# Optimization experiments

Measured on AMD Instinct MI355X. Metric: run time of the kernel, lower is better.

The kernel has to match this reference:

```python
import jax, jax.numpy as jnp
import numpy as np

MEX_C = 2.0 / (np.sqrt(3.0) * np.pi ** 0.25)

def mexican_hat(z):
    return MEX_C * (z * z - 1.0) * jnp.exp(-0.5 * z * z)

def setup_inputs() -> dict:
    key = jax.random.key(0)
    ks = jax.random.split(key, 5)
    B, T, D, O = 4, 2048, 128, 128
    x = jax.random.normal(ks[0], (B, T, D), dtype=jnp.float32)
    # init like torch: scale ~ U(0.5,1.5), translation ~ U(-0.5,0.5), kaiming-ish weights
    scale = jax.random.uniform(ks[1], (O, D), dtype=jnp.float32, minval=0.5, maxval=1.5)
    translation = jax.random.uniform(ks[2], (O, D), dtype=jnp.float32, minval=-0.5, maxval=0.5)
    bound = 1.0 / np.sqrt(D)
    wavelet_weights = jax.random.uniform(ks[3], (O, D), dtype=jnp.float32, minval=-bound, maxval=bound)
    base_w = jax.random.uniform(ks[4], (O, D), dtype=jnp.float32, minval=-bound, maxval=bound)
    ln_gamma = jnp.ones((D,), dtype=jnp.float32)
    ln_beta = jnp.zeros((D,), dtype=jnp.float32)
    return {"x": x, "scale": scale, "translation": translation,
            "wavelet_weights": wavelet_weights, "base_w": base_w,
            "ln_gamma": ln_gamma, "ln_beta": ln_beta}

def reference(x, scale, translation, wavelet_weights, base_w, ln_gamma, ln_beta):
    B, T, D = x.shape
    O = wavelet_weights.shape[0]
    # LayerNorm over last dim (eps = 1e-5, torch default)
    mu = jnp.mean(x, axis=-1, keepdims=True)
    var = jnp.mean((x - mu) ** 2, axis=-1, keepdims=True)
    x_norm = (x - mu) / jnp.sqrt(var + 1e-5) * ln_gamma + ln_beta
    x_flat = x_norm.reshape(B * T, D)                      # (N, D)
    s = jax.nn.softplus(scale) + 0.1                       # (O, D)
    # broadcast intermediate (N, O, D) — the memory-bound path
    z = (x_flat[:, None, :] - translation[None]) / s[None]
    w = jnp.clip(mexican_hat(z), -10.0, 10.0)              # (N, O, D)
    wavelet_out = jnp.einsum('nod,od->no', w, wavelet_weights)
    base_out = x.reshape(B * T, D) @ base_w.T              # base uses raw x
    out = wavelet_out + jax.nn.silu(base_out)
    return out.reshape(B, T, O)
```

## Files before the change

kernel.cpp:

```cpp
#include <hip/hip_runtime.h>


#define D_DIM 128
#define O_DIM 128
#define ROWS  8
#define BLOCK 256
#define CHUNK 16
#define NCHUNK (D_DIM / CHUNK)

#define C1     0.72134752f
#define SQRT_C 0.84932180f
#define WWK    1.2023651f
#define LOG2E  1.44269504f

typedef float v2f __attribute__((ext_vector_type(2)));

__device__ __forceinline__ float4 wk_transform(float sc, float tr, float w_w, float b_w) {
    float sp  = fmaxf(sc, 0.0f) + __logf(1.0f + __expf(-fabsf(sc)));
    float is2 = SQRT_C / (sp + 0.1f);
    float4 w;
    w.x = tr * is2;
    w.y = is2;
    w.z = w_w * WWK;
    w.w = b_w;
    return w;
}

__global__ __launch_bounds__(256) void wavekan_prep(
    const float* __restrict__ scale,
    const float* __restrict__ trans,
    const float* __restrict__ ww,
    const float* __restrict__ bw,
    float4* __restrict__ wsW)
{
    int idx = blockIdx.x * blockDim.x + threadIdx.x;
    if (idx >= O_DIM * D_DIM) return;
    int o = idx >> 7;
    int d = idx & (D_DIM - 1);
    wsW[d * O_DIM + o] = wk_transform(scale[idx], trans[idx], ww[idx], bw[idx]);
}

template<bool USE_WS>
__global__ __launch_bounds__(BLOCK, 4) void wavekan_main(
    const float* __restrict__ x,
    const float* __restrict__ scale,
    const float* __restrict__ trans,
    const float* __restrict__ ww,
    const float* __restrict__ bw,
    const float* __restrict__ gamma,
    const float* __restrict__ beta,
    const float4* __restrict__ wsW,
    float* __restrict__ out,
    int N)
{
    __shared__ float4 s_ln4[D_DIM * 2];
    __shared__ float4 s_rw4[D_DIM * 2];
    __shared__ float4 s_w[CHUNK * O_DIM];

    const int tid  = threadIdx.x;
    const int row0 = blockIdx.x * ROWS;

    {
        const int r  = tid >> 5;
        const int j  = tid & 31;
        const int d0 = j * 4;
        const int grow = row0 + r;

        float4 v4 = make_float4(0.f, 0.f, 0.f, 0.f);
        if (grow < N)
            v4 = *reinterpret_cast<const float4*>(x + (size_t)grow * D_DIM + d0);

        float sum = (v4.x + v4.y) + (v4.z + v4.w);
        float ssq = (v4.x * v4.x + v4.y * v4.y) + (v4.z * v4.z + v4.w * v4.w);
        #pragma unroll
        for (int m = 1; m < 32; m <<= 1) {
            sum += __shfl_xor(sum, m, 64);
            ssq += __shfl_xor(ssq, m, 64);
        }
        const float mean = sum * (1.0f / D_DIM);
        const float var  = ssq * (1.0f / D_DIM) - mean * mean;
        const float rstd = rsqrtf(var + 1e-5f);

        float4 g4 = *reinterpret_cast<const float4*>(gamma + d0);
        float4 b4 = *reinterpret_cast<const float4*>(beta + d0);

        const int q  = r >> 2;
        const int cw = r & 3;
        const int gx = q ^ (j & 1);

        reinterpret_cast<float*>(&s_ln4[(d0 + 0) * 2 + gx])[cw] = (v4.x - mean) * rstd * g4.x + b4.x;
        reinterpret_cast<float*>(&s_ln4[(d0 + 1) * 2 + gx])[cw] = (v4.y - mean) * rstd * g4.y + b4.y;
        reinterpret_cast<float*>(&s_ln4[(d0 + 2) * 2 + gx])[cw] = (v4.z - mean) * rstd * g4.z + b4.z;
        reinterpret_cast<float*>(&s_ln4[(d0 + 3) * 2 + gx])[cw] = (v4.w - mean) * rstd * g4.w + b4.w;
        reinterpret_cast<float*>(&s_rw4[(d0 + 0) * 2 + gx])[cw] = v4.x;
        reinterpret_cast<float*>(&s_rw4[(d0 + 1) * 2 + gx])[cw] = v4.y;
        reinterpret_cast<float*>(&s_rw4[(d0 + 2) * 2 + gx])[cw] = v4.z;
        reinterpret_cast<float*>(&s_rw4[(d0 + 3) * 2 + gx])[cw] = v4.w;
    }

    const int o = tid & (O_DIM - 1);
    const int g = tid >> 7;

    v2f aw0 = {0.f,0.f}, aw1 = {0.f,0.f};
    v2f ab0 = {0.f,0.f}, ab1 = {0.f,0.f};

    for (int c = 0; c < NCHUNK; ++c) {
        __syncthreads();

        if (USE_WS) {
            #pragma unroll
            for (int k = 0; k < (CHUNK * O_DIM) / BLOCK; ++k)
                s_w[k * BLOCK + tid] = wsW[c * (CHUNK * O_DIM) + k * BLOCK + tid];
        } else {
            const int so = tid & 127;
            const int sq = tid >> 7;
            #pragma unroll
            for (int k = 0; k < 8; ++k) {
                const int dloc = sq * 8 + k;
                const int idx  = so * D_DIM + c * CHUNK + dloc;
                s_w[dloc * O_DIM + so] =
                    wk_transform(scale[idx], trans[idx], ww[idx], bw[idx]);
            }
        }
        __syncthreads();

        #pragma unroll
        for (int dl = 0; dl < CHUNK; ++dl) {
            float4 w  = s_w[dl * O_DIM + o];
            const int di = (c * CHUNK + dl) * 2;
            const int gx = g ^ ((dl >> 2) & 1);
            float4 xl = s_ln4[di + gx];
            float4 xr = s_rw4[di + gx];

            v2f u, qq, e;
            u = (v2f){xl.x, xl.y} * w.y - w.x; qq = u * u;
            e = (v2f){__builtin_amdgcn_exp2f(-qq.x), __builtin_amdgcn_exp2f(-qq.y)};
            aw0 += ((qq - C1) * e) * w.z;
            u = (v2f){xl.z, xl.w} * w.y - w.x; qq = u * u;
            e = (v2f){__builtin_amdgcn_exp2f(-qq.x), __builtin_amdgcn_exp2f(-qq.y)};
            aw1 += ((qq - C1) * e) * w.z;

            ab0 += (v2f){xr.x, xr.y} * w.w;
            ab1 += (v2f){xr.z, xr.w} * w.w;
        }
    }

    {
        const int rb = row0 + g * 4;
        float wavv[4]  = {aw0.x, aw0.y, aw1.x, aw1.y};
        float basev[4] = {ab0.x, ab0.y, ab1.x, ab1.y};
        #pragma unroll
        for (int i = 0; i < 4; ++i) {
            if (rb + i < N) {
                float v   = basev[i];
                float sig = 1.0f / (1.0f + __builtin_amdgcn_exp2f(-LOG2E * v));
                out[(size_t)(rb + i) * O_DIM + o] = wavv[i] + v * sig;
            }
        }
    }
}

extern "C" void kernel_launch(void* const* d_in, const int* in_sizes, int n_in,
                              void* d_out, int out_size, void* d_ws, size_t ws_size,
                              hipStream_t stream) {
    const float* x     = (const float*)d_in[0];
    const float* scale = (const float*)d_in[1];
    const float* trans = (const float*)d_in[2];
    const float* ww    = (const float*)d_in[3];
    const float* bw    = (const float*)d_in[4];
    const float* gamma = (const float*)d_in[5];
    const float* beta  = (const float*)d_in[6];
    float* out = (float*)d_out;

    const int N = in_sizes[0] / D_DIM;
    const int grid = (N + ROWS - 1) / ROWS;

    const size_t ws_needed = (size_t)O_DIM * D_DIM * sizeof(float4);
    if (ws_size >= ws_needed) {
        wavekan_prep<<<(O_DIM * D_DIM + 255) / 256, 256, 0, stream>>>(
            scale, trans, ww, bw, (float4*)d_ws);
        wavekan_main<true><<<grid, BLOCK, 0, stream>>>(
            x, scale, trans, ww, bw, gamma, beta, (const float4*)d_ws, out, N);
    } else {
        wavekan_main<false><<<grid, BLOCK, 0, stream>>>(
            x, scale, trans, ww, bw, gamma, beta, nullptr, out, N);
    }
}
```

Before: 101.3 us.

## Hold per-output weights in registers and split D across lanes with shuffle reduction

The main kernel now keeps each thread's slice of transformed weights (32 d-values for one output) in 32 float4 registers, loaded once. It no longer streams weight chunks through shared memory with two barriers per chunk. Each block processes 32 rows with 512 threads: four lane groups split the D dimension and combine partial sums with cross-lane shuffles. The prep kernel now writes weights in a paired layout. This removes repeated LDS weight traffic and syncs, at the cost of high register pressure (launch bounds lowered to 2 blocks per SM), fewer blocks in the grid and an extra reduction per row.

Result: no change. 101.1 us (-0.1%).

```diff
diff --git a/kernel.cpp b/kernel.cpp
--- a/kernel.cpp
+++ b/kernel.cpp
@@ -3,10 +3,9 @@
 
 #define D_DIM 128
 #define O_DIM 128
-#define ROWS  8
-#define BLOCK 256
-#define CHUNK 16
-#define NCHUNK (D_DIM / CHUNK)
+#define ROWS  32
+#define BLOCK 512
+#define XPAD  289
 
 #define C1     0.72134752f
 #define SQRT_C 0.84932180f
@@ -15,15 +14,11 @@
 
 typedef float v2f __attribute__((ext_vector_type(2)));
 
-__device__ __forceinline__ float4 wk_transform(float sc, float tr, float w_w, float b_w) {
+__device__ __forceinline__ void wk_pair(float sc, float tr, float w_w, float b_w,
+                                        float& wx, float& wy, float& wz, float& wb) {
     float sp  = fmaxf(sc, 0.0f) + __logf(1.0f + __expf(-fabsf(sc)));
     float is2 = SQRT_C / (sp + 0.1f);
-    float4 w;
-    w.x = tr * is2;
-    w.y = is2;
-    w.z = w_w * WWK;
-    w.w = b_w;
-    return w;
+    wx = tr * is2; wy = is2; wz = w_w * WWK; wb = b_w;
 }
 
 __global__ __launch_bounds__(256) void wavekan_prep(
@@ -34,14 +29,19 @@
     float4* __restrict__ wsW)
 {
     int idx = blockIdx.x * blockDim.x + threadIdx.x;
-    if (idx >= O_DIM * D_DIM) return;
-    int o = idx >> 7;
-    int d = idx & (D_DIM - 1);
-    wsW[d * O_DIM + o] = wk_transform(scale[idx], trans[idx], ww[idx], bw[idx]);
+    if (idx >= O_DIM * (D_DIM / 2)) return;
+    int o = idx >> 6;
+    int p = idx & 63;
+    int i0 = o * D_DIM + p * 2;
+    float wx0, wy0, wz0, wb0, wx1, wy1, wz1, wb1;
+    wk_pair(scale[i0],     trans[i0],     ww[i0],     bw[i0],     wx0, wy0, wz0, wb0);
+    wk_pair(scale[i0 + 1], trans[i0 + 1], ww[i0 + 1], bw[i0 + 1], wx1, wy1, wz1, wb1);
+    wsW[(p * O_DIM + o) * 2 + 0] = make_float4(wx0, wx1, wy0, wy1);
+    wsW[(p * O_DIM + o) * 2 + 1] = make_float4(wz0, wz1, wb0, wb1);
 }
 
 template<bool USE_WS>
-__global__ __launch_bounds__(BLOCK, 4) void wavekan_main(
+__global__ __launch_bounds__(BLOCK, 2) void wavekan_main(
     const float* __restrict__ x,
     const float* __restrict__ scale,
     const float* __restrict__ trans,
@@ -53,27 +53,53 @@
     float* __restrict__ out,
     int N)
 {
-    __shared__ float4 s_ln4[D_DIM * 2];
-    __shared__ float4 s_rw4[D_DIM * 2];
-    __shared__ float4 s_w[CHUNK * O_DIM];
+    __shared__ float4 s_ln4[4 * XPAD];
+    __shared__ float4 s_rw4[4 * XPAD];
 
     const int tid  = threadIdx.x;
+    const int lane = tid & 63;
+    const int wv   = tid >> 6;
+    const int o    = wv * 16 + (lane & 15);
+    const int dg   = lane >> 4;
     const int row0 = blockIdx.x * ROWS;
 
+    float4 wA[16], wB[16];
+    if (USE_WS) {
+        #pragma unroll
+        for (int k = 0; k < 16; ++k) {
+            const int p = dg * 16 + k;
+            wA[k] = wsW[(p * O_DIM + o) * 2 + 0];
+            wB[k] = wsW[(p * O_DIM + o) * 2 + 1];
+        }
+    } else {
+        #pragma unroll
+        for (int k = 0; k < 16; ++k) {
+            const int i0 = o * D_DIM + dg * 32 + 2 * k;
+            float wx0, wy0, wz0, wb0, wx1, wy1, wz1, wb1;
+            wk_pair(scale[i0],     trans[i0],     ww[i0],     bw[i0],     wx0, wy0, wz0, wb0);
+            wk_pair(scale[i0 + 1], trans[i0 + 1], ww[i0 + 1], bw[i0 + 1], wx1, wy1, wz1, wb1);
+            wA[k] = make_float4(wx0, wx1, wy0, wy1);
+            wB[k] = make_float4(wz0, wz1, wb0, wb1);
+        }
+    }
+
     {
-        const int r  = tid >> 5;
-        const int j  = tid & 31;
-        const int d0 = j * 4;
+        const int r    = tid >> 4;
+        const int j    = tid & 15;
+        const int d0   = j * 8;
         const int grow = row0 + r;
 
-        float4 v4 = make_float4(0.f, 0.f, 0.f, 0.f);
-        if (grow < N)
-            v4 = *reinterpret_cast<const float4*>(x + (size_t)grow * D_DIM + d0);
-
-        float sum = (v4.x + v4.y) + (v4.z + v4.w);
-        float ssq = (v4.x * v4.x + v4.y * v4.y) + (v4.z * v4.z + v4.w * v4.w);
+        float4 va = make_float4(0.f, 0.f, 0.f, 0.f);
+        float4 vb = make_float4(0.f, 0.f, 0.f, 0.f);
+        if (grow < N) {
+            va = *reinterpret_cast<const float4*>(x + (size_t)grow * D_DIM + d0);
+            vb = *reinterpret_cast<const float4*>(x + (size_t)grow * D_DIM + d0 + 4);
+        }
+        float sum = ((va.x + va.y) + (va.z + va.w)) + ((vb.x + vb.y) + (vb.z + vb.w));
+        float ssq = ((va.x * va.x + va.y * va.y) + (va.z * va.z + va.w * va.w))
+                  + ((vb.x * vb.x + vb.y * vb.y) + (vb.z * vb.z + vb.w * vb.w));
         #pragma unroll
-        for (int m = 1; m < 32; m <<= 1) {
+        for (int m = 1; m < 16; m <<= 1) {
             sum += __shfl_xor(sum, m, 64);
             ssq += __shfl_xor(ssq, m, 64);
         }
@@ -81,81 +107,63 @@
         const float var  = ssq * (1.0f / D_DIM) - mean * mean;
         const float rstd = rsqrtf(var + 1e-5f);
 
-        float4 g4 = *reinterpret_cast<const float4*>(gamma + d0);
-        float4 b4 = *reinterpret_cast<const float4*>(beta + d0);
+        float4 ga = *reinterpret_cast<const float4*>(gamma + d0);
+        float4 gb = *reinterpret_cast<const float4*>(gamma + d0 + 4);
+        float4 ba = *reinterpret_cast<const float4*>(beta + d0);
+        float4 bb = *reinterpret_cast<const float4*>(beta + d0 + 4);
 
-        const int q  = r >> 2;
-        const int cw = r & 3;
-        const int gx = q ^ (j & 1);
+        const int wdg = j >> 2;
+        const int q0  = (j & 3) * 2;
+        const int ib  = wdg * XPAD + r * 9 + q0;
 
-        reinterpret_cast<float*>(&s_ln4[(d0 + 0) * 2 + gx])[cw] = (v4.x - mean) * rstd * g4.x + b4.x;
-        reinterpret_cast<float*>(&s_ln4[(d0 + 1) * 2 + gx])[cw] = (v4.y - mean) * rstd * g4.y + b4.y;
-        reinterpret_cast<float*>(&s_ln4[(d0 + 2) * 2 + gx])[cw] = (v4.z - mean) * rstd * g4.z + b4.z;
-        reinterpret_cast<float*>(&s_ln4[(d0 + 3) * 2 + gx])[cw] = (v4.w - mean) * rstd * g4.w + b4.w;
-        reinterpret_cast<float*>(&s_rw4[(d0 + 0) * 2 + gx])[cw] = v4.x;
-        reinterpret_cast<float*>(&s_rw4[(d0 + 1) * 2 + gx])[cw] = v4.y;
-        reinterpret_cast<float*>(&s_rw4[(d0 + 2) * 2 + gx])[cw] = v4.z;
-        reinterpret_cast<float*>(&s_rw4[(d0 + 3) * 2 + gx])[cw] = v4.w;
+        s_ln4[ib]     = make_float4((va.x - mean) * rstd * ga.x + ba.x,
+                                    (va.y - mean) * rstd * ga.y + ba.y,
+                                    (va.z - mean) * rstd * ga.z + ba.z,
+                                    (va.w - mean) * rstd * ga.w + ba.w);
+        s_ln4[ib + 1] = make_float4((vb.x - mean) * rstd * gb.x + bb.x,
+                                    (vb.y - mean) * rstd * gb.y + bb.y,
+                                    (vb.z - mean) * rstd * gb.z + bb.z,
+                                    (vb.w - mean) * rstd * gb.w + bb.w);
+        s_rw4[ib]     = va;
+        s_rw4[ib + 1] = vb;
     }
+    __syncthreads();
 
-    const int o = tid & (O_DIM - 1);
-    const int g = tid >> 7;
-
-    v2f aw0 = {0.f,0.f}, aw1 = {0.f,0.f};
-    v2f ab0 = {0.f,0.f}, ab1 = {0.f,0.f};
-
-    for (int c = 0; c < NCHUNK; ++c) {
-        __syncthreads();
-
-        if (USE_WS) {
-            #pragma unroll
-            for (int k = 0; k < (CHUNK * O_DIM) / BLOCK; ++k)
-                s_w[k * BLOCK + tid] = wsW[c * (CHUNK * O_DIM) + k * BLOCK + tid];
-        } else {
-            const int so = tid & 127;
-            const int sq = tid >> 7;
-            #pragma unroll
-            for (int k = 0; k < 8; ++k) {
-                const int dloc = sq * 8 + k;
-                const int idx  = so * D_DIM + c * CHUNK + dloc;
-                s_w[dloc * O_DIM + so] =
-                    wk_transform(scale[idx], trans[idx], ww[idx], bw[idx]);
-            }
-        }
-        __syncthreads();
-
+    #pragma unroll 1
+    for (int r = 0; r < ROWS; ++r) {
+        const int xb = dg * XPAD + r * 9;
+        v2f aw = {0.f, 0.f};
+        v2f ab = {0.f, 0.f};
         #pragma unroll
-        for (int dl = 0; dl < CHUNK; ++dl) {
-            float4 w  = s_w[dl * O_DIM + o];
-            const int di = (c * CHUNK + dl) * 2;
-            const int gx = g ^ ((dl >> 2) & 1);
-            float4 xl = s_ln4[di + gx];
-            float4 xr = s_rw4[di + gx];
+        for (int k4 = 0; k4 < 8; ++k4) {
+            float4 xl = s_ln4[xb + k4];
+            float4 xr = s_rw4[xb + k4];
+            float4 a0 = wA[2 * k4],     b0 = wB[2 * k4];
+            float4 a1 = wA[2 * k4 + 1], b1 = wB[2 * k4 + 1];
 
             v2f u, qq, e;
-            u = (v2f){xl.x, xl.y} * w.y - w.x; qq = u * u;
-            e = (v2f){__builtin_amdgcn_exp2f(-qq.x), __builtin_amdgcn_exp2f(-qq.y)};
-            aw0 += ((qq - C1) * e) * w.z;
-            u = (v2f){xl.z, xl.w} * w.y - w.x; qq = u * u;
-            e = (v2f){__builtin_amdgcn_exp2f(-qq.x), __builtin_amdgcn_exp2f(-qq.y)};
-            aw1 += ((qq - C1) * e) * w.z;
+            u  = (v2f){xl.x, xl.y} * (v2f){a0.z, a0.w} - (v2f){a0.x, a0.y};
+            qq = u * u;
+            e  = (v2f){__builtin_amdgcn_exp2f(-qq.x), __builtin_amdgcn_exp2f(-qq.y)};
+            aw += ((qq - C1) * e) * (v2f){b0.x, b0.y};
+            ab += (v2f){xr.x, xr.y} * (v2f){b0.z, b0.w};
 
-            ab0 += (v2f){xr.x, xr.y} * w.w;
-            ab1 += (v2f){xr.z, xr.w} * w.w;
+            u  = (v2f){xl.z, xl.w} * (v2f){a1.z, a1.w} - (v2f){a1.x, a1.y};
+            qq = u * u;
+            e  = (v2f){__builtin_amdgcn_exp2f(-qq.x), __builtin_amdgcn_exp2f(-qq.y)};
+            aw += ((qq - C1) * e) * (v2f){b1.x, b1.y};
+            ab += (v2f){xr.z, xr.w} * (v2f){b1.z, b1.w};
         }
-    }
+        float wav = aw.x + aw.y;
+        float bas = ab.x + ab.y;
+        wav += __shfl_xor(wav, 16, 64);
+        wav += __shfl_xor(wav, 32, 64);
+        bas += __shfl_xor(bas, 16, 64);
+        bas += __shfl_xor(bas, 32, 64);
 
-    {
-        const int rb = row0 + g * 4;
-        float wavv[4]  = {aw0.x, aw0.y, aw1.x, aw1.y};
-        float basev[4] = {ab0.x, ab0.y, ab1.x, ab1.y};
-        #pragma unroll
-        for (int i = 0; i < 4; ++i) {
-            if (rb + i < N) {
-                float v   = basev[i];
-                float sig = 1.0f / (1.0f + __builtin_amdgcn_exp2f(-LOG2E * v));
-                out[(size_t)(rb + i) * O_DIM + o] = wavv[i] + v * sig;
-            }
+        if ((lane < 16) && (row0 + r < N)) {
+            float sig = 1.0f / (1.0f + __builtin_amdgcn_exp2f(-LOG2E * bas));
+            out[(size_t)(row0 + r) * O_DIM + o] = wav + bas * sig;
         }
     }
 }
@@ -175,9 +183,9 @@
     const int N = in_sizes[0] / D_DIM;
     const int grid = (N + ROWS - 1) / ROWS;
 
-    const size_t ws_needed = (size_t)O_DIM * D_DIM * sizeof(float4);
+    const size_t ws_needed = (size_t)O_DIM * (D_DIM / 2) * 2 * sizeof(float4);
     if (ws_size >= ws_needed) {
-        wavekan_prep<<<(O_DIM * D_DIM + 255) / 256, 256, 0, stream>>>(
+        wavekan_prep<<<(O_DIM * (D_DIM / 2) + 255) / 256, 256, 0, stream>>>(
             scale, trans, ww, bw, (float4*)d_ws);
         wavekan_main<true><<<grid, BLOCK, 0, stream>>>(
             x, scale, trans, ww, bw, gamma, beta, (const float4*)d_ws, out, N);
```
